# Kernel optimization log

Measured on AMD Instinct MI355X. Metric: run time of the kernel, lower is better.

Reference implementation:

```python
import jax, jax.numpy as jnp
import numpy as np

N_USER = 1_000_000
N_ITEM = 100_000
E = 16          # embedding_size
O = 16          # out_size per head
H = 4           # head_num
HID = 32        # hidden_size
B = 8192        # batch
S = 200         # sample_num
L = 50          # history length
NSUPP = 50_000  # supp_user_num


def _xavier(key, shape):
    fan_in, fan_out = shape[-2], shape[-1]
    std = np.sqrt(2.0 / (fan_in + fan_out))
    return (jax.random.normal(key, shape) * std).astype(jnp.float32)


def setup_inputs() -> dict:
    key = jax.random.key(0)
    ks = jax.random.split(key, 16)
    uid = jax.random.randint(ks[0], (B,), 0, N_USER)
    iid = jax.random.randint(ks[1], (B,), 0, N_ITEM)
    return {
        "user_embedding": _xavier(ks[2], (N_USER, E)),
        "item_embedding": _xavier(ks[3], (N_ITEM, E)),
        "wq": _xavier(ks[4], (H, E, O)),   # per-head Wq (no bias)
        "wk": _xavier(ks[5], (H, E, O)),
        "wv": _xavier(ks[6], (H, O, O)),
        "w_out": _xavier(ks[7], (H * O, O)),
        "l1_w": _xavier(ks[8], (3 * E, HID)),
        "l1_b": jnp.full((HID,), 0.1, jnp.float32),
        "l2_w": _xavier(ks[9], (HID, HID // 2)),
        "l2_b": jnp.full((HID // 2,), 0.1, jnp.float32),
        "l3_w": _xavier(ks[10], (HID // 2, 1)),
        "l3_b": jnp.full((1,), 0.1, jnp.float32),
        "user_bias": jnp.zeros((N_USER, 1), jnp.float32),
        "item_bias": jnp.zeros((N_ITEM, 1), jnp.float32),
        "x": jnp.stack([uid, iid], axis=1),                          # [B,2]
        "history": jax.random.randint(ks[11], (B, L), 0, N_ITEM),    # [B,L]
        "history_len": jax.random.randint(ks[12], (B,), 1, L + 1),   # [B] >=1
        "supp_users": jax.random.randint(ks[13], (NSUPP,), 0, N_USER),
        "sample_index": jax.random.randint(ks[14], (H, B, S), 0, NSUPP),
    }


def reference(user_embedding, item_embedding, wq, wk, wv, w_out,
              l1_w, l1_b, l2_w, l2_b, l3_w, l3_b, user_bias, item_bias,
              x, history, history_len, supp_users, sample_index):
    user_id = x[:, 0]
    item_id = x[:, 1]

    # user init embedding = mean-by-len of full (unmasked) history, as in source
    hist_emb = item_embedding[history]                                # [B,L,E]
    user_init = hist_emb.sum(axis=1) / history_len[:, None].astype(jnp.float32)  # [B,E]

    # per-head GAT over sampled support users (all heads vectorized)
    nb = user_embedding[supp_users[sample_index]]                     # [H,B,S,E]
    q = jnp.einsum('be,heo->hbo', user_init, wq)                      # [H,B,O]
    k = jnp.einsum('hbse,heo->hbso', nb, wk)                          # [H,B,S,O]
    attn = jax.nn.softmax(jnp.einsum('hbo,hbso->hbs', q, k), axis=-1)
    ctx = jnp.einsum('hbs,hbso->hbo', attn, k)                        # [H,B,O]
    gat = jnp.einsum('hbo,hop->hbp', ctx, wv)                         # [H,B,O]
    gat = jnp.transpose(gat, (1, 0, 2)).reshape(B, H * O)             # concat heads

    user_emb = gat @ w_out                                            # [B,O]
    item_emb = item_embedding[item_id]                                # [B,E]
    interaction = user_emb * item_emb
    ratings = interaction.sum(axis=1)

    h = jnp.concatenate([user_emb, item_emb, interaction], axis=1)    # [B,3E]
    x1 = jnp.tanh(h @ l1_w + l1_b)
    x2 = jnp.tanh(x1 @ l2_w + l2_b)
    x3 = (x2 @ l3_w + l3_b).reshape(-1)

    ub = user_bias[user_id, 0]
    ib = item_bias[item_id, 0]
    return (ratings + x3) / 2.0 + ub + ib
```

## Files before the change

### kernel.cpp

```cpp
#include <hip/hip_runtime.h>
#include <math.h>

#define N_USERS 1000000
#define N_ITEMS 100000
#define EMB 16
#define OUTD 16
#define NH 4
#define HID 32
#define BB 8192
#define SS 200
#define LL 50
#define NSUPP 50000

#define SLICE_ROWS 1536
#define NP 33
#define TBL_ROWS (NP * SLICE_ROWS)
#define SLICE_BYTES (SLICE_ROWS * EMB * 2)
#define GBB 32

typedef float v4f __attribute__((ext_vector_type(4)));
typedef _Float16 h2 __attribute__((ext_vector_type(2)));
typedef _Float16 h8 __attribute__((ext_vector_type(8)));

#define WAVE_SYNC() do { asm volatile("s_waitcnt lgkmcnt(0)" ::: "memory"); \
                         __builtin_amdgcn_sched_barrier(0); } while (0)

__global__ __launch_bounds__(256) void prep_kernel(
    const float* __restrict__ user_emb,
    const int*   __restrict__ supp_users,
    const float* __restrict__ wk,
    const float* __restrict__ wq,
    const float* __restrict__ wv,
    const float* __restrict__ item_emb,
    const int*   __restrict__ history,
    const int*   __restrict__ history_len,
    _Float16*    __restrict__ tbl,
    _Float16*    __restrict__ qtbuf,
    float*       __restrict__ Wkv)
{
    __shared__ float s_ui[4][EMB];
    __shared__ float s_wq[NH * EMB * OUTD];
    __shared__ float s_wk[NH * EMB * OUTD];
    __shared__ float s_q[4][NH * OUTD];

    int t = threadIdx.x;
    if (blockIdx.x < NSUPP / 16) {
        int n0 = blockIdx.x * 16;
        int ul = t >> 4, e = t & 15;
        int row = supp_users[n0 + ul];
        tbl[(size_t)(n0 + ul) * EMB + e] =
            (_Float16)user_emb[(size_t)row * EMB + e];
    } else if (blockIdx.x < NSUPP / 16 + BB / 4) {
        for (int i = t; i < NH * EMB * OUTD; i += 256) {
            s_wq[i] = wq[i];
            s_wk[i] = wk[i];
        }
        int g    = t >> 6;
        int lane = t & 63;
        int l4   = lane >> 4;
        int e    = lane & 15;
        int b    = (blockIdx.x - NSUPP / 16) * 4 + g;

        float sum = 0.f;
        for (int l = l4; l < LL; l += 4) {
            int it = __builtin_nontemporal_load(history + (size_t)b * LL + l);
            sum += item_emb[(size_t)it * EMB + e];
        }
        sum += __shfl_xor(sum, 16);
        sum += __shfl_xor(sum, 32);
        if (lane < EMB) s_ui[g][lane] = sum / (float)history_len[b];
        __syncthreads();

        int h = (t >> 4) & 3;
        int o = t & 15;
        float acc = 0.f;
#pragma unroll
        for (int ee = 0; ee < EMB; ++ee)
            acc += s_ui[g][ee] * s_wq[(h * EMB + ee) * OUTD + o];
        s_q[g][h * OUTD + o] = acc;
        __syncthreads();

        float qt = 0.f;
#pragma unroll
        for (int oo = 0; oo < OUTD; ++oo)
            qt += s_wk[(h * EMB + o) * OUTD + oo] * s_q[g][h * OUTD + oo];
        qtbuf[((size_t)b * NH + h) * EMB + o] = (_Float16)qt;
    } else {
        for (int i = t; i < NH * EMB * OUTD; i += 256) {
            int h = i >> 8, e = (i >> 4) & 15, p = i & 15;
            float a = 0.f;
#pragma unroll
            for (int o = 0; o < OUTD; ++o)
                a += wk[(h * EMB + e) * OUTD + o] * wv[(h * OUTD + o) * OUTD + p];
            Wkv[i] = a;
        }
    }
}

__global__ __launch_bounds__(512, 2) void attn_kernel(
    const _Float16* __restrict__ tbl,
    const _Float16* __restrict__ qtbuf,
    const int*   __restrict__ sample_index,
    const float* __restrict__ Wkv,
    float*       __restrict__ gat)
{
    __shared__ __align__(16) _Float16 s_slice[2][SLICE_ROWS * EMB];
    __shared__ unsigned short s_list[128 * SS];
    __shared__ unsigned char  s_cnt[128][36];
    __shared__ unsigned int   s_hist[8][40];

    int tid  = threadIdx.x;
    int wave = tid >> 6;
    int lane = tid & 63;
    int g    = lane >> 2;
    int qt   = lane & 3;
    int hb   = wave * 16 + g;
    int h    = hb & 3;
    int bl   = hb >> 2;
    int bfull = blockIdx.x * GBB + bl;

    v4f stg[6];
#pragma unroll
    for (int i = 0; i < 6; ++i)
        stg[i] = *(const v4f*)((const char*)tbl + (size_t)i * 8192 + (size_t)tid * 16);

    for (int bs = 0; bs < 16; ++bs) {
        int hbs = wave * 16 + bs;
        int hs = hbs & 3, bls = hbs >> 2;
        const int* si = sample_index + ((size_t)hs * BB + (blockIdx.x * GBB + bls)) * SS;
        int v0 = __builtin_nontemporal_load(si + lane);
        int v1 = __builtin_nontemporal_load(si + lane + 64);
        int v2 = __builtin_nontemporal_load(si + lane + 128);
        int v3 = (lane < SS - 192) ? __builtin_nontemporal_load(si + lane + 192) : -1;

        if (lane < NP + 1) s_hist[wave][lane] = 0;
        WAVE_SYNC();
        int b0 = ((v0 >> 9) * 21846) >> 16;
        int b1 = ((v1 >> 9) * 21846) >> 16;
        int b2 = ((v2 >> 9) * 21846) >> 16;
        int b3 = (v3 >= 0) ? (((v3 >> 9) * 21846) >> 16) : 0;
        atomicAdd(&s_hist[wave][b0], 1u);
        atomicAdd(&s_hist[wave][b1], 1u);
        atomicAdd(&s_hist[wave][b2], 1u);
        if (v3 >= 0) atomicAdd(&s_hist[wave][b3], 1u);
        WAVE_SYNC();
        if (lane == 0) {
            unsigned run = 0;
            for (int k = 0; k < NP; ++k) {
                unsigned c = s_hist[wave][k];
                s_cnt[hbs][k] = (unsigned char)c;
                s_hist[wave][k] = run;
                run += c;
            }
        }
        WAVE_SYNC();
        unsigned p0 = atomicAdd(&s_hist[wave][b0], 1u);
        s_list[hbs * SS + p0] = (unsigned short)v0;
        unsigned p1 = atomicAdd(&s_hist[wave][b1], 1u);
        s_list[hbs * SS + p1] = (unsigned short)v1;
        unsigned p2 = atomicAdd(&s_hist[wave][b2], 1u);
        s_list[hbs * SS + p2] = (unsigned short)v2;
        if (v3 >= 0) {
            unsigned p3 = atomicAdd(&s_hist[wave][b3], 1u);
            s_list[hbs * SS + p3] = (unsigned short)v3;
        }
        WAVE_SYNC();
    }

    const h8* qtp = (const h8*)(qtbuf + ((size_t)bfull * NH + h) * EMB);
    h8 qA = qtp[0], qB = qtp[1];
    h2 tq0 = __builtin_shufflevector(qA, qA, 0, 1);
    h2 tq1 = __builtin_shufflevector(qA, qA, 2, 3);
    h2 tq2 = __builtin_shufflevector(qA, qA, 4, 5);
    h2 tq3 = __builtin_shufflevector(qA, qA, 6, 7);
    h2 tq4 = __builtin_shufflevector(qB, qB, 0, 1);
    h2 tq5 = __builtin_shufflevector(qB, qB, 2, 3);
    h2 tq6 = __builtin_shufflevector(qB, qB, 4, 5);
    h2 tq7 = __builtin_shufflevector(qB, qB, 6, 7);

#pragma unroll
    for (int i = 0; i < 6; ++i)
        *(v4f*)((char*)&s_slice[0][0] + (size_t)i * 8192 + (size_t)tid * 16) = stg[i];
    __syncthreads();

    float l = 0.f;
    float cu[16];
#pragma unroll
    for (int j = 0; j < 16; ++j) cu[j] = 0.f;
    int base = 0;

    for (int p = 0; p < NP; ++p) {
        if (p + 1 < NP) {
            size_t sb = (size_t)(p + 1) * SLICE_BYTES;
#pragma unroll
            for (int i = 0; i < 6; ++i)
                stg[i] = *(const v4f*)((const char*)tbl + sb + (size_t)i * 8192
                                        + (size_t)tid * 16);
        }
        const h8* sl = (const h8*)&s_slice[p & 1][0];
        int cnt = (int)s_cnt[hb][p];
        int pbase = p * SLICE_ROWS;

        for (int it = 0;; ++it) {
            int off = it * 4 + qt;
            bool valid = off < cnt;
            if (__ballot(valid) == 0ull) break;
            int pos = valid ? base + off : 0;
            int v   = (int)s_list[hb * SS + pos];
            int rl  = valid ? v - pbase : 0;
            h8 u0 = sl[rl * 2];
            h8 u1 = sl[rl * 2 + 1];
            h2 a0 = __builtin_shufflevector(u0, u0, 0, 1);
            h2 a1 = __builtin_shufflevector(u0, u0, 2, 3);
            h2 a2 = __builtin_shufflevector(u0, u0, 4, 5);
            h2 a3 = __builtin_shufflevector(u0, u0, 6, 7);
            h2 a4 = __builtin_shufflevector(u1, u1, 0, 1);
            h2 a5 = __builtin_shufflevector(u1, u1, 2, 3);
            h2 a6 = __builtin_shufflevector(u1, u1, 4, 5);
            h2 a7 = __builtin_shufflevector(u1, u1, 6, 7);
            float s = __builtin_amdgcn_fdot2(a0, tq0,
                      __builtin_amdgcn_fdot2(a1, tq1,
                      __builtin_amdgcn_fdot2(a2, tq2,
                      __builtin_amdgcn_fdot2(a3, tq3,
                      __builtin_amdgcn_fdot2(a4, tq4,
                      __builtin_amdgcn_fdot2(a5, tq5,
                      __builtin_amdgcn_fdot2(a6, tq6,
                      __builtin_amdgcn_fdot2(a7, tq7,
                      0.f, false), false), false), false),
                      false), false), false), false);
            float w = valid ? __expf(s) : 0.f;
            l += w;
#pragma unroll
            for (int j = 0; j < 8; ++j) cu[j]     += w * (float)u0[j];
#pragma unroll
            for (int j = 0; j < 8; ++j) cu[8 + j] += w * (float)u1[j];
        }
        base += cnt;
        __syncthreads();
        if (p + 1 < NP) {
#pragma unroll
            for (int i = 0; i < 6; ++i)
                *(v4f*)((char*)&s_slice[(p + 1) & 1][0] + (size_t)i * 8192
                        + (size_t)tid * 16) = stg[i];
        }
        __syncthreads();
    }

    l += __shfl_xor(l, 1);
    l += __shfl_xor(l, 2);
#pragma unroll
    for (int j = 0; j < 16; ++j) {
        cu[j] += __shfl_xor(cu[j], 1);
        cu[j] += __shfl_xor(cu[j], 2);
    }
    float inv = 1.f / l;
    v4f acc = {0.f, 0.f, 0.f, 0.f};
#pragma unroll
    for (int e = 0; e < EMB; ++e)
        acc += cu[e] * *(const v4f*)(Wkv + ((size_t)(h * EMB + e) * OUTD) + qt * 4);
    acc *= inv;
    *(v4f*)(gat + (size_t)bfull * (NH * OUTD) + h * OUTD + qt * 4) = acc;
}

__global__ __launch_bounds__(256) void epilogue_kernel(
    const float* __restrict__ gat,
    const float* __restrict__ item_emb,
    const float* __restrict__ w_out,
    const float* __restrict__ l1_w, const float* __restrict__ l1_b,
    const float* __restrict__ l2_w, const float* __restrict__ l2_b,
    const float* __restrict__ l3_w, const float* __restrict__ l3_b,
    const float* __restrict__ user_bias, const float* __restrict__ item_bias,
    const int*   __restrict__ x,
    float*       __restrict__ out)
{
    int t    = threadIdx.x;
    int g    = t >> 6;
    int lane = t & 63;
    int b    = blockIdx.x * 4 + g;

    __shared__ float s_gat[4][NH * OUTD];
    __shared__ float s_ue[4][OUTD];
    __shared__ float s_ie[4][EMB];
    __shared__ float s_x1[4][HID];
    __shared__ float s_x2[4][HID / 2];

    int uid = x[(size_t)b * 2 + 0];
    int iid = x[(size_t)b * 2 + 1];

    s_gat[g][lane] = gat[(size_t)b * (NH * OUTD) + lane];
    if (lane < EMB) s_ie[g][lane] = item_emb[(size_t)iid * EMB + lane];
    __syncthreads();

    if (lane < OUTD) {
        float acc = 0.f;
#pragma unroll
        for (int j = 0; j < NH * OUTD; ++j) acc += s_gat[g][j] * w_out[j * OUTD + lane];
        s_ue[g][lane] = acc;
    }
    __syncthreads();

    if (lane < HID) {
        float acc = l1_b[lane];
#pragma unroll
        for (int i = 0; i < EMB; ++i) {
            float ue = s_ue[g][i], ie = s_ie[g][i];
            acc += ue * l1_w[i * HID + lane]
                 + ie * l1_w[(EMB + i) * HID + lane]
                 + ue * ie * l1_w[(2 * EMB + i) * HID + lane];
        }
        s_x1[g][lane] = tanhf(acc);
    }
    __syncthreads();

    if (lane < HID / 2) {
        float acc = l2_b[lane];
#pragma unroll
        for (int j = 0; j < HID; ++j) acc += s_x1[g][j] * l2_w[j * (HID / 2) + lane];
        s_x2[g][lane] = tanhf(acc);
    }
    __syncthreads();

    if (lane == 0) {
        float x3 = l3_b[0];
#pragma unroll
        for (int j = 0; j < HID / 2; ++j) x3 += s_x2[g][j] * l3_w[j];
        float ratings = 0.f;
#pragma unroll
        for (int o = 0; o < OUTD; ++o) ratings += s_ue[g][o] * s_ie[g][o];
        out[b] = 0.5f * (ratings + x3) + user_bias[uid] + item_bias[iid];
    }
}

extern "C" void kernel_launch(void* const* d_in, const int* in_sizes, int n_in,
                              void* d_out, int out_size, void* d_ws, size_t ws_size,
                              hipStream_t stream) {
    const float* user_embedding = (const float*)d_in[0];
    const float* item_embedding = (const float*)d_in[1];
    const float* wq             = (const float*)d_in[2];
    const float* wk             = (const float*)d_in[3];
    const float* wv             = (const float*)d_in[4];
    const float* w_out          = (const float*)d_in[5];
    const float* l1_w           = (const float*)d_in[6];
    const float* l1_b           = (const float*)d_in[7];
    const float* l2_w           = (const float*)d_in[8];
    const float* l2_b           = (const float*)d_in[9];
    const float* l3_w           = (const float*)d_in[10];
    const float* l3_b           = (const float*)d_in[11];
    const float* user_bias      = (const float*)d_in[12];
    const float* item_bias      = (const float*)d_in[13];
    const int*   x              = (const int*)d_in[14];
    const int*   history        = (const int*)d_in[15];
    const int*   history_len    = (const int*)d_in[16];
    const int*   supp_users     = (const int*)d_in[17];
    const int*   sample_index   = (const int*)d_in[18];
    float* out = (float*)d_out;

    char* ws = (char*)d_ws;
    _Float16* tbl = (_Float16*)ws;
    ws += (size_t)TBL_ROWS * EMB * sizeof(_Float16);
    _Float16* qtbuf = (_Float16*)ws;
    ws += (size_t)BB * NH * EMB * sizeof(_Float16);
    float* gat = (float*)ws;
    ws += (size_t)BB * NH * OUTD * sizeof(float);
    float* Wkv = (float*)ws;

    prep_kernel<<<NSUPP / 16 + BB / 4 + 1, 256, 0, stream>>>(
        user_embedding, supp_users, wk, wq, wv,
        item_embedding, history, history_len, tbl, qtbuf, Wkv);
    attn_kernel<<<BB / GBB, 512, 0, stream>>>(tbl, qtbuf, sample_index, Wkv, gat);
    epilogue_kernel<<<BB / 4, 256, 0, stream>>>(
        gat, item_embedding, w_out, l1_w, l1_b, l2_w, l2_b, l3_w, l3_b,
        user_bias, item_bias, x, out);
}
```

Measured before the change: 243.0 us.

## Software-pipeline attention inner loop and parallelize per-slice prefix scan

The serial lane-0 prefix sum over slice counts becomes a wave-wide shuffle scan that stores exclusive offsets. The inner gather/accumulate loop is software-pipelined: each iteration prefetches the next index and row from LDS while computing the current one. The trip count is a precomputed max across the wave instead of a ballot each iteration, and the dot product is split into two shorter dependency chains. Launch bounds drop from 2 blocks per CU to 1, giving the compiler more registers for the pipelined state at the cost of possibly lower occupancy.

```diff
diff --git a/kernel.cpp b/kernel.cpp
--- a/kernel.cpp
+++ b/kernel.cpp
@@ -97,7 +97,7 @@
     }
 }
 
-__global__ __launch_bounds__(512, 2) void attn_kernel(
+__global__ __launch_bounds__(512, 1) void attn_kernel(
     const _Float16* __restrict__ tbl,
     const _Float16* __restrict__ qtbuf,
     const int*   __restrict__ sample_index,
@@ -106,7 +106,7 @@
 {
     __shared__ __align__(16) _Float16 s_slice[2][SLICE_ROWS * EMB];
     __shared__ unsigned short s_list[128 * SS];
-    __shared__ unsigned char  s_cnt[128][36];
+    __shared__ unsigned short s_ofs[128][NP + 1];
     __shared__ unsigned int   s_hist[8][40];
 
     int tid  = threadIdx.x;
@@ -133,7 +133,7 @@
         int v2 = __builtin_nontemporal_load(si + lane + 128);
         int v3 = (lane < SS - 192) ? __builtin_nontemporal_load(si + lane + 192) : -1;
 
-        if (lane < NP + 1) s_hist[wave][lane] = 0;
+        if (lane < NP) s_hist[wave][lane] = 0;
         WAVE_SYNC();
         int b0 = ((v0 >> 9) * 21846) >> 16;
         int b1 = ((v1 >> 9) * 21846) >> 16;
@@ -144,15 +144,19 @@
         atomicAdd(&s_hist[wave][b2], 1u);
         if (v3 >= 0) atomicAdd(&s_hist[wave][b3], 1u);
         WAVE_SYNC();
-        if (lane == 0) {
-            unsigned run = 0;
-            for (int k = 0; k < NP; ++k) {
-                unsigned c = s_hist[wave][k];
-                s_cnt[hbs][k] = (unsigned char)c;
-                s_hist[wave][k] = run;
-                run += c;
-            }
-        }
+        unsigned c = (lane < NP) ? s_hist[wave][lane] : 0;
+        unsigned sc = c;
+#pragma unroll
+        for (int d = 1; d < 64; d <<= 1) {
+            unsigned tu = (unsigned)__shfl_up((int)sc, d, 64);
+            if (lane >= d) sc += tu;
+        }
+        unsigned excl = sc - c;
+        if (lane < NP) {
+            s_hist[wave][lane] = excl;
+            s_ofs[hbs][lane] = (unsigned short)excl;
+        }
+        if (lane == NP) s_ofs[hbs][NP] = (unsigned short)SS;
         WAVE_SYNC();
         unsigned p0 = atomicAdd(&s_hist[wave][b0], 1u);
         s_list[hbs * SS + p0] = (unsigned short)v0;
@@ -198,42 +202,59 @@
                                         + (size_t)tid * 16);
         }
         const h8* sl = (const h8*)&s_slice[p & 1][0];
-        int cnt = (int)s_cnt[hb][p];
         int pbase = p * SLICE_ROWS;
-
-        for (int it = 0;; ++it) {
-            int off = it * 4 + qt;
-            bool valid = off < cnt;
-            if (__ballot(valid) == 0ull) break;
-            int pos = valid ? base + off : 0;
-            int v   = (int)s_list[hb * SS + pos];
-            int rl  = valid ? v - pbase : 0;
-            h8 u0 = sl[rl * 2];
-            h8 u1 = sl[rl * 2 + 1];
-            h2 a0 = __builtin_shufflevector(u0, u0, 0, 1);
-            h2 a1 = __builtin_shufflevector(u0, u0, 2, 3);
-            h2 a2 = __builtin_shufflevector(u0, u0, 4, 5);
-            h2 a3 = __builtin_shufflevector(u0, u0, 6, 7);
-            h2 a4 = __builtin_shufflevector(u1, u1, 0, 1);
-            h2 a5 = __builtin_shufflevector(u1, u1, 2, 3);
-            h2 a6 = __builtin_shufflevector(u1, u1, 4, 5);
-            h2 a7 = __builtin_shufflevector(u1, u1, 6, 7);
-            float s = __builtin_amdgcn_fdot2(a0, tq0,
-                      __builtin_amdgcn_fdot2(a1, tq1,
-                      __builtin_amdgcn_fdot2(a2, tq2,
-                      __builtin_amdgcn_fdot2(a3, tq3,
-                      __builtin_amdgcn_fdot2(a4, tq4,
-                      __builtin_amdgcn_fdot2(a5, tq5,
-                      __builtin_amdgcn_fdot2(a6, tq6,
-                      __builtin_amdgcn_fdot2(a7, tq7,
-                      0.f, false), false), false), false),
-                      false), false), false), false);
-            float w = valid ? __expf(s) : 0.f;
-            l += w;
-#pragma unroll
-            for (int j = 0; j < 8; ++j) cu[j]     += w * (float)u0[j];
-#pragma unroll
-            for (int j = 0; j < 8; ++j) cu[8 + j] += w * (float)u1[j];
+        int cnt = (int)s_ofs[hb][p + 1] - base;
+        int mx = (cnt + 3) >> 2;
+        mx = max(mx, __shfl_xor(mx, 4));
+        mx = max(mx, __shfl_xor(mx, 8));
+        mx = max(mx, __shfl_xor(mx, 16));
+        mx = max(mx, __shfl_xor(mx, 32));
+        const int lbase = hb * SS + base;
+
+        if (mx > 0) {
+            int offA = qt;
+            bool vA  = offA < cnt;
+            int idxA = (int)s_list[lbase + (vA ? offA : 0)];
+            int offB = qt + 4;
+            bool vB  = offB < cnt;
+            int idxB = (int)s_list[lbase + (vB ? offB : 0)];
+            int rlA  = vA ? idxA - pbase : 0;
+            h8 uA0 = sl[rlA * 2];
+            h8 uA1 = sl[rlA * 2 + 1];
+            for (int it = 0; it < mx; ++it) {
+                int rlB = vB ? idxB - pbase : 0;
+                h8 uB0 = sl[rlB * 2];
+                h8 uB1 = sl[rlB * 2 + 1];
+                int offC = offB + 4;
+                bool vC  = offC < cnt;
+                int idxC = (int)s_list[lbase + (vC ? offC : 0)];
+                h2 a0 = __builtin_shufflevector(uA0, uA0, 0, 1);
+                h2 a1 = __builtin_shufflevector(uA0, uA0, 2, 3);
+                h2 a2 = __builtin_shufflevector(uA0, uA0, 4, 5);
+                h2 a3 = __builtin_shufflevector(uA0, uA0, 6, 7);
+                h2 a4 = __builtin_shufflevector(uA1, uA1, 0, 1);
+                h2 a5 = __builtin_shufflevector(uA1, uA1, 2, 3);
+                h2 a6 = __builtin_shufflevector(uA1, uA1, 4, 5);
+                h2 a7 = __builtin_shufflevector(uA1, uA1, 6, 7);
+                float sx = __builtin_amdgcn_fdot2(a0, tq0,
+                           __builtin_amdgcn_fdot2(a1, tq1,
+                           __builtin_amdgcn_fdot2(a2, tq2,
+                           __builtin_amdgcn_fdot2(a3, tq3, 0.f, false),
+                           false), false), false);
+                float sy = __builtin_amdgcn_fdot2(a4, tq4,
+                           __builtin_amdgcn_fdot2(a5, tq5,
+                           __builtin_amdgcn_fdot2(a6, tq6,
+                           __builtin_amdgcn_fdot2(a7, tq7, 0.f, false),
+                           false), false), false);
+                float w = vA ? __expf(sx + sy) : 0.f;
+                l += w;
+#pragma unroll
+                for (int j = 0; j < 8; ++j) cu[j]     += w * (float)uA0[j];
+#pragma unroll
+                for (int j = 0; j < 8; ++j) cu[8 + j] += w * (float)uA1[j];
+                offA = offB; vA = vB; uA0 = uB0; uA1 = uB1;
+                offB = offC; vB = vC; idxB = idxC;
+            }
         }
         base += cnt;
         __syncthreads();
```

After: 243.6 us. About the same (+0.2%).
